# Kernel optimization log

Measured on AMD Instinct MI355X. Metric: run time of the kernel, lower is better.

Reference implementation:

```python
import jax, jax.numpy as jnp
from jax import lax
import numpy as np

K = 3        # kernel_size
PAD = 1      # zero padding applied to x before sampling
STRIDE = 1   # stride of the offset-predicting conv
B, C_IN, C_OUT, H, W = 8, 64, 64, 64, 64
N = K * K


def setup_inputs() -> dict:
    key = jax.random.key(0)
    k1, k2, k3 = jax.random.split(key, 3)
    x = jax.random.normal(k1, (B, C_IN, H, W), jnp.float32)
    W_off = jax.random.normal(k2, (2 * N, C_IN, 3, 3), jnp.float32) * 0.05
    b_off = jnp.zeros((2 * N,), jnp.float32)
    W_conv = jax.random.normal(k3, (C_OUT, C_IN, K, K), jnp.float32) * 0.05
    return {"x": x, "W_off": W_off, "b_off": b_off, "W_conv": W_conv}


def _deform_conv(x, W_off, b_off, W_conv):
    # offset conv: Conv2d(C_IN, 2*N, 3, padding=1, stride=STRIDE) with bias
    offset = lax.conv_general_dilated(
        x, W_off, (STRIDE, STRIDE), ((1, 1), (1, 1)),
        dimension_numbers=("NCHW", "OIHW", "NCHW")) + b_off[None, :, None, None]
    b, _, h, w = offset.shape

    # zero-pad input (nn.ZeroPad2d(PAD))
    xp = jnp.pad(x, ((0, 0), (0, 0), (PAD, PAD), (PAD, PAD)))
    Hp, Wp = xp.shape[2], xp.shape[3]

    # p_0: output-pixel base coords (1-based, stride-spaced), shape (h, w)
    p0x = jnp.arange(1, h * STRIDE + 1, STRIDE, dtype=x.dtype)[:, None] * jnp.ones((1, w), x.dtype)
    p0y = jnp.ones((h, 1), x.dtype) * jnp.arange(1, w * STRIDE + 1, STRIDE, dtype=x.dtype)[None, :]
    # p_n: kernel-relative offsets, flattened in 'ij' meshgrid order, shape (N,)
    kk = jnp.arange(-(K - 1) // 2, (K - 1) // 2 + 1, dtype=x.dtype)
    pnx = jnp.repeat(kk, K)
    pny = jnp.tile(kk, K)

    off = offset.transpose(0, 2, 3, 1)  # (b, h, w, 2N)
    px = p0x[None, :, :, None] + pnx[None, None, None, :] + off[..., :N]  # (b,h,w,N)
    py = p0y[None, :, :, None] + pny[None, None, None, :] + off[..., N:]

    # integer corners from detached p (p.detach().floor() in torch)
    pxd = lax.stop_gradient(px)
    pyd = lax.stop_gradient(py)
    qlt_x = jnp.clip(jnp.floor(pxd), 0, Hp - 1).astype(jnp.int32)
    qlt_y = jnp.clip(jnp.floor(pyd), 0, Wp - 1).astype(jnp.int32)
    qrb_x = jnp.clip(jnp.floor(pxd) + 1, 0, Hp - 1).astype(jnp.int32)
    qrb_y = jnp.clip(jnp.floor(pyd) + 1, 0, Wp - 1).astype(jnp.int32)

    # clamp p (differentiable)
    pxc = jnp.clip(px, 0, Hp - 1)
    pyc = jnp.clip(py, 0, Wp - 1)

    flt_x = qlt_x.astype(x.dtype); flt_y = qlt_y.astype(x.dtype)
    frb_x = qrb_x.astype(x.dtype); frb_y = qrb_y.astype(x.dtype)
    g_lt = (1 + (flt_x - pxc)) * (1 + (flt_y - pyc))
    g_rb = (1 - (frb_x - pxc)) * (1 - (frb_y - pyc))
    g_lb = (1 + (flt_x - pxc)) * (1 - (frb_y - pyc))  # q_lb = (qlt_x, qrb_y)
    g_rt = (1 - (frb_x - pxc)) * (1 + (flt_y - pyc))  # q_rt = (qrb_x, qlt_y)

    # gather: per-batch fancy indexing, (c,Hp,Wp)[:,qx,qy] -> (c,h,w,N)
    gather = jax.vmap(lambda xb, qx, qy: xb[:, qx, qy])
    x_lt = gather(xp, qlt_x, qlt_y)
    x_rb = gather(xp, qrb_x, qrb_y)
    x_lb = gather(xp, qlt_x, qrb_y)
    x_rt = gather(xp, qrb_x, qlt_y)

    xo = (g_lt[:, None] * x_lt + g_rb[:, None] * x_rb
          + g_lb[:, None] * x_lb + g_rt[:, None] * x_rt)  # (b,c,h,w,N)

    # reshape_x_offset: (b,c,h,w,kh*kw) -> (b,c,h*kh,w*kw)
    c = xo.shape[1]
    xo = xo.reshape(b, c, h, w, K, K).transpose(0, 1, 2, 4, 3, 5).reshape(b, c, h * K, w * K)

    # final conv: kernel K, stride K, no bias
    return lax.conv_general_dilated(
        xo, W_conv, (K, K), ((0, 0), (0, 0)),
        dimension_numbers=("NCHW", "OIHW", "NCHW"))


def reference(x, W_off, b_off, W_conv):
    return _deform_conv(x, W_off, b_off, W_conv)
```

## Files before the change

### kernel.cpp

```cpp
#include <hip/hip_runtime.h>
#include <hip/hip_bf16.h>


typedef unsigned int u32;
typedef unsigned short u16;
typedef short s8v __attribute__((ext_vector_type(8)));
typedef short s4v __attribute__((ext_vector_type(4)));
typedef float f4v __attribute__((ext_vector_type(4)));

#define XOS_STRIDE 592

__device__ __forceinline__ u16 f2bf(float f) {
  u32 u = __builtin_bit_cast(u32, f);
  u32 r = (u + 0x7FFFu + ((u >> 16) & 1u)) >> 16;
  return (u16)r;
}

__device__ __forceinline__ f4v bf2f4(s4v v) {
  f4v r;
  r[0] = __builtin_bit_cast(float, ((u32)(u16)v[0]) << 16);
  r[1] = __builtin_bit_cast(float, ((u32)(u16)v[1]) << 16);
  r[2] = __builtin_bit_cast(float, ((u32)(u16)v[2]) << 16);
  r[3] = __builtin_bit_cast(float, ((u32)(u16)v[3]) << 16);
  return r;
}

__global__ __launch_bounds__(256) void k01(
    const float* __restrict__ x,
    const float* __restrict__ wconv,
    const float* __restrict__ woff,
    u16* __restrict__ wfrag,
    u16* __restrict__ wofrag,
    u16* __restrict__ xT) {
  __shared__ float tile[64][65];
  int bid = blockIdx.x;
  int t = threadIdx.x;
  int tid = bid * 256 + t;

  if (tid < 4608) {
    int nt = tid / 1152, ks = (tid / 64) % 18, lane = tid & 63;
    int co = nt * 16 + (lane & 15);
    int n = ks >> 1, s = ks & 1;
    int cl8 = (lane >> 4) << 3;
    u16* dst = wfrag + tid * 8;
    #pragma unroll
    for (int j = 0; j < 8; ++j) {
      int c = s * 32 + cl8 + j;
      dst[j] = f2bf(wconv[co * 576 + c * 9 + n]);
    }
  }
  if (tid >= 8192 && tid < 10496) {
    int idx = tid - 8192;
    int nt2 = idx / 1152, ks = (idx / 64) % 18, lane = idx & 63;
    int o = nt2 * 16 + (lane & 15);
    int n = ks >> 1, s = ks & 1;
    int cl8 = (lane >> 4) << 3;
    u16* dst = wofrag + idx * 8;
    #pragma unroll
    for (int j = 0; j < 8; ++j) {
      int c = s * 32 + cl8 + j;
      float v = (o < 18) ? woff[(o * 64 + c) * 9 + n] : 0.f;
      dst[j] = f2bf(v);
    }
  }

  int bh = ((bid & 7) << 6) | (bid >> 3);
  const float* xb = x + (bh >> 6) * 262144 + (bh & 63) * 64;
  int w = t & 63, cr = t >> 6;
  #pragma unroll
  for (int i = 0; i < 16; ++i) {
    int c = cr * 16 + i;
    tile[c][w] = xb[c * 4096 + w];
  }
  __syncthreads();
  u32* dstT = (u32*)(xT + bh * 4096);
  int c2 = t & 31, wr = t >> 5;
  #pragma unroll
  for (int i = 0; i < 8; ++i) {
    int w2 = wr * 8 + i;
    u32 lo = f2bf(tile[c2 * 2][w2]);
    u32 hi = f2bf(tile[c2 * 2 + 1][w2]);
    dstT[w2 * 32 + c2] = lo | (hi << 16);
  }
}

__global__ __launch_bounds__(256, 4) void k2_sample(
    const u16*  __restrict__ xT,
    const u16*  __restrict__ wfrag,
    const u16*  __restrict__ wofrag,
    const float* __restrict__ boff,
    float* __restrict__ out) {
  __shared__ __align__(16) u16 xim[16 * XOS_STRIDE];
  __shared__ float offs_lds[288];

  int bid = blockIdx.x;
  int b = bid & 7;
  int r = bid >> 3;
  int h = r >> 2, wq = r & 3;
  int t = threadIdx.x;
  int cg4 = t & 15;
  int wls = t >> 4;
  int w_g = wq * 16 + wls;
  const u16* xTb = xT + b * 262144;

  {
    const u16* xq = xTb + cg4 * 4;
    u16* xrow = xim + wls * XOS_STRIDE + cg4 * 4;
    #pragma unroll
    for (int n = 0; n < 9; ++n) {
      int hh = h + (n / 3) - 1;
      int ww = w_g + (n % 3) - 1;
      s4v v = {0, 0, 0, 0};
      if (hh >= 0 && hh < 64 && ww >= 0 && ww < 64)
        v = *(const s4v*)(xq + (hh * 64 + ww) * 64);
      *(s4v*)(xrow + n * 64) = v;
    }
  }
  __syncthreads();

  if (t < 64) {
    int lane = t;
    int aoff = (lane & 15) * XOS_STRIDE + ((lane >> 4) << 3);
    const s8v* Wo = (const s8v*)wofrag;
    f4v a0 = {0.f, 0.f, 0.f, 0.f}, a1 = {0.f, 0.f, 0.f, 0.f};
    #pragma unroll
    for (int ks = 0; ks < 18; ++ks) {
      s8v a  = *(const s8v*)(xim + aoff + ks * 32);
      a0 = __builtin_amdgcn_mfma_f32_16x16x32_bf16(a, Wo[ks * 64 + lane], a0, 0, 0, 0);
      a1 = __builtin_amdgcn_mfma_f32_16x16x32_bf16(a, Wo[(18 + ks) * 64 + lane], a1, 0, 0, 0);
    }
    int quad = lane >> 4, ol = lane & 15;
    float bo0 = boff[ol];
    #pragma unroll
    for (int r4 = 0; r4 < 4; ++r4)
      offs_lds[ol * 16 + quad * 4 + r4] = a0[r4] + bo0;
    if (ol < 2) {
      float bo1 = boff[16 + ol];
      #pragma unroll
      for (int r4 = 0; r4 < 4; ++r4)
        offs_lds[(16 + ol) * 16 + quad * 4 + r4] = a1[r4] + bo1;
    }
  }
  __syncthreads();

  u32 qa[9];
  f4v gg[9];
  {
    #pragma unroll
    for (int n = 0; n < 9; ++n) {
      float ox = offs_lds[n * 16 + wls];
      float oy = offs_lds[(9 + n) * 16 + wls];
      float px = (float)(h + (n / 3)) + ox;
      float py = (float)(w_g + (n % 3)) + oy;
      float fx = floorf(px), fy = floorf(py);
      float pxc  = fminf(fmaxf(px, 0.f), 65.f);
      float pyc  = fminf(fmaxf(py, 0.f), 65.f);
      float fltx = fminf(fmaxf(fx, 0.f), 65.f);
      float flty = fminf(fmaxf(fy, 0.f), 65.f);
      float frbx = fminf(fmaxf(fx + 1.f, 0.f), 65.f);
      float frby = fminf(fmaxf(fy + 1.f, 0.f), 65.f);
      float ax = 1.f + fltx - pxc, bx = 1.f - frbx + pxc;
      float ay = 1.f + flty - pyc, by = 1.f - frby + pyc;
      float glt = ax * ay, grb = bx * by, glb = ax * by, grt = bx * ay;

      int ilt = (int)fltx, jlt = (int)flty, irb = (int)frbx, jrb = (int)frby;
      bool bi0 = (ilt >= 1 && ilt <= 64), bj0 = (jlt >= 1 && jlt <= 64);
      bool bi1 = (irb >= 1 && irb <= 64), bj1 = (jrb >= 1 && jrb <= 64);
      u32 i0 = bi0 ? (u32)(ilt - 1) : 0u;
      u32 j0 = bj0 ? (u32)(jlt - 1) : 0u;
      u32 i1 = bi1 ? (u32)(irb - 1) : 0u;
      u32 j1 = bj1 ? (u32)(jrb - 1) : 0u;
      qa[n] = i0 | (j0 << 8) | (i1 << 16) | (j1 << 24);
      f4v gv;
      gv[0] = (bi0 && bj0) ? glt : 0.f;
      gv[1] = (bi1 && bj1) ? grb : 0.f;
      gv[2] = (bi0 && bj1) ? glb : 0.f;
      gv[3] = (bi1 && bj0) ? grt : 0.f;
      gg[n] = gv;
    }
  }
  {
    const u16* xq = xTb + cg4 * 4;
    u16* xrow = xim + wls * XOS_STRIDE + cg4 * 4;
    #pragma unroll
    for (int n = 0; n < 9; ++n) {
      u32 q = qa[n];
      f4v g = gg[n];
      int i0 = (int)(q & 255u) << 12;
      int j0 = (int)((q >> 8) & 255u) << 6;
      int i1 = (int)((q >> 16) & 255u) << 12;
      int j1 = (int)(q >> 24) << 6;
      f4v lt = bf2f4(*(const s4v*)(xq + i0 + j0));
      f4v rb = bf2f4(*(const s4v*)(xq + i1 + j1));
      f4v lb = bf2f4(*(const s4v*)(xq + i0 + j1));
      f4v rt = bf2f4(*(const s4v*)(xq + i1 + j0));
      f4v v  = g[0] * lt + g[1] * rb + g[2] * lb + g[3] * rt;
      s4v pk;
      pk[0] = (short)f2bf(v[0]);
      pk[1] = (short)f2bf(v[1]);
      pk[2] = (short)f2bf(v[2]);
      pk[3] = (short)f2bf(v[3]);
      *(s4v*)(xrow + n * 64) = pk;
    }
  }
  __syncthreads();

  {
    int wv = t >> 6;
    int lane = t & 63;
    int aoff = (lane & 15) * XOS_STRIDE + ((lane >> 4) << 3);
    const s8v* Wf = (const s8v*)wfrag;
    f4v acc = {0.f, 0.f, 0.f, 0.f};
    #pragma unroll
    for (int ks = 0; ks < 18; ++ks) {
      s8v a  = *(const s8v*)(xim + aoff + ks * 32);
      s8v b0 = Wf[(wv * 18 + ks) * 64 + lane];
      acc = __builtin_amdgcn_mfma_f32_16x16x32_bf16(a, b0, acc, 0, 0, 0);
    }
    int quad = lane >> 4;
    int co = wv * 16 + (lane & 15);
    *(f4v*)(out + b * 262144 + co * 4096 + h * 64 + wq * 16 + quad * 4) = acc;
  }
}

extern "C" void kernel_launch(void* const* d_in, const int* in_sizes, int n_in,
                              void* d_out, int out_size, void* d_ws, size_t ws_size,
                              hipStream_t stream) {
  const float *x = nullptr, *woff = nullptr, *boff = nullptr, *wconv = nullptr;
  for (int i = 0; i < n_in; ++i) {
    switch (in_sizes[i]) {
      case 2097152: x     = (const float*)d_in[i]; break;
      case 10368:   woff  = (const float*)d_in[i]; break;
      case 18:      boff  = (const float*)d_in[i]; break;
      case 36864:   wconv = (const float*)d_in[i]; break;
      default: break;
    }
  }
  if (!x)     x     = (const float*)d_in[0];
  if (!woff)  woff  = (const float*)d_in[1];
  if (!boff)  boff  = (const float*)d_in[2];
  if (!wconv) wconv = (const float*)d_in[3];
  float* out = (float*)d_out;

  u16* wfrag  = (u16*)d_ws;
  u16* wofrag = (u16*)((char*)d_ws + 73728);
  u16* xT     = (u16*)((char*)d_ws + 131072);

  k01<<<512, 256, 0, stream>>>(x, wconv, woff, wfrag, wofrag, xT);
  k2_sample<<<2048, 256, 0, stream>>>(xT, wfrag, wofrag, boff, out);
}
```

Before: 93.79 us.

## Process 32 output pixels per block to reuse weight fragments across two tiles

```diff
diff --git a/kernel.cpp b/kernel.cpp
--- a/kernel.cpp
+++ b/kernel.cpp
@@ -8,7 +8,7 @@
 typedef short s4v __attribute__((ext_vector_type(4)));
 typedef float f4v __attribute__((ext_vector_type(4)));
 
-#define XOS_STRIDE 592
+#define XOS_STRIDE 584
 
 __device__ __forceinline__ u16 f2bf(float f) {
   u32 u = __builtin_bit_cast(u32, f);
@@ -90,22 +90,24 @@
     const u16*  __restrict__ wofrag,
     const float* __restrict__ boff,
     float* __restrict__ out) {
-  __shared__ __align__(16) u16 xim[16 * XOS_STRIDE];
-  __shared__ float offs_lds[288];
+  __shared__ __align__(16) u16 xim[32 * XOS_STRIDE];
+  __shared__ float offs_lds[576];
 
   int bid = blockIdx.x;
   int b = bid & 7;
   int r = bid >> 3;
-  int h = r >> 2, wq = r & 3;
+  int h = r >> 1, wh = r & 1;
   int t = threadIdx.x;
   int cg4 = t & 15;
   int wls = t >> 4;
-  int w_g = wq * 16 + wls;
   const u16* xTb = xT + b * 262144;
 
-  {
+  #pragma unroll
+  for (int it = 0; it < 2; ++it) {
+    int wl = wls + 16 * it;
+    int w_g = wh * 32 + wl;
     const u16* xq = xTb + cg4 * 4;
-    u16* xrow = xim + wls * XOS_STRIDE + cg4 * 4;
+    u16* xrow = xim + wl * XOS_STRIDE + cg4 * 4;
     #pragma unroll
     for (int n = 0; n < 9; ++n) {
       int hh = h + (n / 3) - 1;
@@ -118,38 +120,44 @@
   }
   __syncthreads();
 
-  if (t < 64) {
-    int lane = t;
-    int aoff = (lane & 15) * XOS_STRIDE + ((lane >> 4) << 3);
-    const s8v* Wo = (const s8v*)wofrag;
-    f4v a0 = {0.f, 0.f, 0.f, 0.f}, a1 = {0.f, 0.f, 0.f, 0.f};
-    #pragma unroll
-    for (int ks = 0; ks < 18; ++ks) {
-      s8v a  = *(const s8v*)(xim + aoff + ks * 32);
-      a0 = __builtin_amdgcn_mfma_f32_16x16x32_bf16(a, Wo[ks * 64 + lane], a0, 0, 0, 0);
-      a1 = __builtin_amdgcn_mfma_f32_16x16x32_bf16(a, Wo[(18 + ks) * 64 + lane], a1, 0, 0, 0);
-    }
-    int quad = lane >> 4, ol = lane & 15;
-    float bo0 = boff[ol];
-    #pragma unroll
-    for (int r4 = 0; r4 < 4; ++r4)
-      offs_lds[ol * 16 + quad * 4 + r4] = a0[r4] + bo0;
-    if (ol < 2) {
-      float bo1 = boff[16 + ol];
+  {
+    int wv = t >> 6;
+    int lane = t & 63;
+    if (wv < 2) {
+      int aoff = ((lane & 15) + 16 * wv) * XOS_STRIDE + ((lane >> 4) << 3);
+      const s8v* Wo = (const s8v*)wofrag;
+      f4v a0 = {0.f, 0.f, 0.f, 0.f}, a1 = {0.f, 0.f, 0.f, 0.f};
+      #pragma unroll
+      for (int ks = 0; ks < 18; ++ks) {
+        s8v a  = *(const s8v*)(xim + aoff + ks * 32);
+        a0 = __builtin_amdgcn_mfma_f32_16x16x32_bf16(a, Wo[ks * 64 + lane], a0, 0, 0, 0);
+        a1 = __builtin_amdgcn_mfma_f32_16x16x32_bf16(a, Wo[(18 + ks) * 64 + lane], a1, 0, 0, 0);
+      }
+      int quad = lane >> 4, ol = lane & 15;
+      float bo0 = boff[ol];
       #pragma unroll
       for (int r4 = 0; r4 < 4; ++r4)
-        offs_lds[(16 + ol) * 16 + quad * 4 + r4] = a1[r4] + bo1;
-    }
-  }
-  __syncthreads();
-
-  u32 qa[9];
-  f4v gg[9];
-  {
+        offs_lds[ol * 32 + wv * 16 + quad * 4 + r4] = a0[r4] + bo0;
+      if (ol < 2) {
+        float bo1 = boff[16 + ol];
+        #pragma unroll
+        for (int r4 = 0; r4 < 4; ++r4)
+          offs_lds[(16 + ol) * 32 + wv * 16 + quad * 4 + r4] = a1[r4] + bo1;
+      }
+    }
+  }
+  __syncthreads();
+
+  #pragma unroll
+  for (int it = 0; it < 2; ++it) {
+    int wl = wls + 16 * it;
+    int w_g = wh * 32 + wl;
+    u32 qa[9];
+    f4v gg[9];
     #pragma unroll
     for (int n = 0; n < 9; ++n) {
-      float ox = offs_lds[n * 16 + wls];
-      float oy = offs_lds[(9 + n) * 16 + wls];
+      float ox = offs_lds[n * 32 + wl];
+      float oy = offs_lds[(9 + n) * 32 + wl];
       float px = (float)(h + (n / 3)) + ox;
       float py = (float)(w_g + (n % 3)) + oy;
       float fx = floorf(px), fy = floorf(py);
@@ -178,10 +186,8 @@
       gv[3] = (bi1 && bj0) ? grt : 0.f;
       gg[n] = gv;
     }
-  }
-  {
     const u16* xq = xTb + cg4 * 4;
-    u16* xrow = xim + wls * XOS_STRIDE + cg4 * 4;
+    u16* xrow = xim + wl * XOS_STRIDE + cg4 * 4;
     #pragma unroll
     for (int n = 0; n < 9; ++n) {
       u32 q = qa[n];
@@ -208,18 +214,23 @@
   {
     int wv = t >> 6;
     int lane = t & 63;
-    int aoff = (lane & 15) * XOS_STRIDE + ((lane >> 4) << 3);
+    int aoff0 = (lane & 15) * XOS_STRIDE + ((lane >> 4) << 3);
+    int aoff1 = aoff0 + 16 * XOS_STRIDE;
     const s8v* Wf = (const s8v*)wfrag;
-    f4v acc = {0.f, 0.f, 0.f, 0.f};
+    f4v acc0 = {0.f, 0.f, 0.f, 0.f}, acc1 = {0.f, 0.f, 0.f, 0.f};
     #pragma unroll
     for (int ks = 0; ks < 18; ++ks) {
-      s8v a  = *(const s8v*)(xim + aoff + ks * 32);
       s8v b0 = Wf[(wv * 18 + ks) * 64 + lane];
-      acc = __builtin_amdgcn_mfma_f32_16x16x32_bf16(a, b0, acc, 0, 0, 0);
+      s8v a0 = *(const s8v*)(xim + aoff0 + ks * 32);
+      s8v a1 = *(const s8v*)(xim + aoff1 + ks * 32);
+      acc0 = __builtin_amdgcn_mfma_f32_16x16x32_bf16(a0, b0, acc0, 0, 0, 0);
+      acc1 = __builtin_amdgcn_mfma_f32_16x16x32_bf16(a1, b0, acc1, 0, 0, 0);
     }
     int quad = lane >> 4;
     int co = wv * 16 + (lane & 15);
-    *(f4v*)(out + b * 262144 + co * 4096 + h * 64 + wq * 16 + quad * 4) = acc;
+    float* ob = out + b * 262144 + co * 4096 + h * 64 + wh * 32;
+    *(f4v*)(ob + quad * 4)      = acc0;
+    *(f4v*)(ob + 16 + quad * 4) = acc1;
   }
 }
 
@@ -247,5 +258,5 @@
   u16* xT     = (u16*)((char*)d_ws + 131072);
 
   k01<<<512, 256, 0, stream>>>(x, wconv, woff, wfrag, wofrag, xT);
-  k2_sample<<<2048, 256, 0, stream>>>(xT, wfrag, wofrag, boff, out);
-}
+  k2_sample<<<1024, 256, 0, stream>>>(xT, wfrag, wofrag, boff, out);
+}
```

Result: no change. 92.16 us (-1.7%).
